# Kernel tuning notes

Measured on AMD Instinct MI355X. Metric: run time of the kernel, lower is better.

Reference implementation:

```python
import jax, jax.numpy as jnp
import numpy as np

B, T, H, K = 16, 8192, 256, 128
HQ = H // 4
NEG_INF = -jnp.inf


def setup_inputs() -> dict:
    key = jax.random.key(0)
    k1, k2, k3, k4, k5, k6, k7 = jax.random.split(key, 7)
    projected = jax.random.normal(k1, (B, T, H), dtype=jnp.float32)
    boundaries = jnp.sort(jax.random.randint(k2, (B, K, 2), 0, T), axis=-1)
    slot_mask = jax.random.randint(k3, (B, K), 0, 2, dtype=jnp.int32)
    # score_fn params: Linear(H, H//4) -> Tanh -> Linear(H//4, 1)
    s1 = 1.0 / np.sqrt(H)
    s2 = 1.0 / np.sqrt(HQ)
    W1 = jax.random.uniform(k4, (H, HQ), jnp.float32, -s1, s1)
    b1 = jax.random.uniform(k5, (HQ,), jnp.float32, -s1, s1)
    W2 = jax.random.uniform(k6, (HQ, 1), jnp.float32, -s2, s2)
    b2 = jax.random.uniform(k7, (1,), jnp.float32, -s2, s2)
    return {"projected": projected, "boundaries": boundaries, "slot_mask": slot_mask,
            "W1": W1, "b1": b1, "W2": W2, "b2": b2}


def reference(projected, boundaries, slot_mask, W1, b1, W2, b2):
    # scores: [B, T]
    h = jnp.tanh(projected @ W1 + b1)          # [B,T,HQ]
    scores = (h @ W2 + b2)[..., 0]             # [B,T]

    tidx = jnp.arange(T)[None, :, None]         # [1,T,1]
    starts = boundaries[:, None, :, 0]          # [B,1,K]
    ends = boundaries[:, None, :, 1]            # [B,1,K]
    in_slot = (tidx >= starts) & (tidx < ends) & (slot_mask[:, None, :] > 0)  # [B,T,K]

    # masked softmax over T, safe for fully-masked slots (torch yields 0 via masked_fill)
    s = scores[:, :, None]                      # [B,T,1] broadcast over K
    m = jnp.max(jnp.where(in_slot, s, NEG_INF), axis=1, keepdims=True)  # [B,1,K]
    m_safe = jnp.where(jnp.isfinite(m), m, 0.0)
    num = jnp.where(in_slot, jnp.exp(s - m_safe), 0.0)                  # [B,T,K]
    den = jnp.sum(num, axis=1, keepdims=True)                           # [B,1,K]
    w = num / jnp.where(den > 0, den, 1.0)                              # [B,T,K]

    return jnp.einsum('btk,bth->bkh', w, projected)                     # [B,K,H]
```

## Files before the change

kernel.cpp:

```cpp
#include <hip/hip_runtime.h>
#include <hip/hip_bf16.h>

#define BB 16
#define TT 8192
#define HH 256
#define KK 128
#define HQ 64

#define PT 64

typedef __attribute__((ext_vector_type(8))) short short8;
typedef __attribute__((ext_vector_type(4))) float f32x4;

__device__ inline unsigned short bf16_rne(float f) {
  unsigned u = __float_as_uint(f);
  unsigned r = u + 0x7FFF + ((u >> 16) & 1);
  return (unsigned short)(r >> 16);
}
__device__ inline float bf16_to_f(unsigned short h) {
  return __uint_as_float(((unsigned)h) << 16);
}

__global__ void prep_kernel(const float* __restrict__ W1,
                            unsigned short* __restrict__ Wp)
{
  int f = blockIdx.x * 256 + threadIdx.x;
  int e = f & 7;
  int l = (f >> 3) & 63;
  int n = (f >> 9) & 3;
  int s = f >> 11;
  int k = s * 32 + ((l >> 4) * 8) + e;
  int j = n * 16 + (l & 15);
  float w = W1[k * HQ + j];
  unsigned short hi = bf16_rne(w);
  Wp[f] = hi;
  Wp[16384 + f] = bf16_rne(w - bf16_to_f(hi));
}

__global__ __launch_bounds__(256, 2) void scores_mfma_kernel(
    const float* __restrict__ proj, const unsigned short* __restrict__ Wp,
    const float* __restrict__ b1, const float* __restrict__ W2,
    const float* __restrict__ b2, float* __restrict__ scores)
{
  __shared__ unsigned short Ahi[64][264];
  __shared__ unsigned short Alo[64][264];
  __shared__ float part[4][64];

  const int tid = threadIdx.x;
  const long long tile = blockIdx.x;
  const float4* src4 = (const float4*)(proj + tile * (64LL * HH));

  #pragma unroll
  for (int r = 0; r < 16; ++r) {
    int f = r * 256 + tid;
    int t = f >> 6;
    int c = f & 63;
    float4 v = src4[f];
    unsigned short h0 = bf16_rne(v.x), h1 = bf16_rne(v.y);
    unsigned short h2 = bf16_rne(v.z), h3 = bf16_rne(v.w);
    *(ushort4*)&Ahi[t][4 * c] = make_ushort4(h0, h1, h2, h3);
    *(ushort4*)&Alo[t][4 * c] = make_ushort4(bf16_rne(v.x - bf16_to_f(h0)),
                                             bf16_rne(v.y - bf16_to_f(h1)),
                                             bf16_rne(v.z - bf16_to_f(h2)),
                                             bf16_rne(v.w - bf16_to_f(h3)));
  }
  __syncthreads();

  const int w = tid >> 6;
  const int l = tid & 63;
  const int g = l >> 4;
  const int c = l & 15;

  f32x4 acc[4];
  #pragma unroll
  for (int m = 0; m < 4; ++m) acc[m] = (f32x4){0.f, 0.f, 0.f, 0.f};

  const short8* wp_hi = (const short8*)Wp;
  const short8* wp_lo = (const short8*)(Wp + 16384);

  #pragma unroll
  for (int s = 0; s < 8; ++s) {
    short8 bhi = wp_hi[(s * 4 + w) * 64 + l];
    short8 blo = wp_lo[(s * 4 + w) * 64 + l];
    #pragma unroll
    for (int m = 0; m < 4; ++m) {
      short8 ahi = *(const short8*)&Ahi[m * 16 + c][s * 32 + g * 8];
      short8 alo = *(const short8*)&Alo[m * 16 + c][s * 32 + g * 8];
      acc[m] = __builtin_amdgcn_mfma_f32_16x16x32_bf16(ahi, bhi, acc[m], 0, 0, 0);
      acc[m] = __builtin_amdgcn_mfma_f32_16x16x32_bf16(ahi, blo, acc[m], 0, 0, 0);
      acc[m] = __builtin_amdgcn_mfma_f32_16x16x32_bf16(alo, bhi, acc[m], 0, 0, 0);
    }
  }

  const int j = w * 16 + c;
  const float b1j = b1[j];
  const float w2j = W2[j];

  #pragma unroll
  for (int m = 0; m < 4; ++m) {
    #pragma unroll
    for (int r = 0; r < 4; ++r) {
      float x = tanhf(acc[m][r] + b1j) * w2j;
      x += __shfl_xor(x, 1);
      x += __shfl_xor(x, 2);
      x += __shfl_xor(x, 4);
      x += __shfl_xor(x, 8);
      if (c == r) part[w][m * 16 + g * 4 + r] = x;
    }
  }
  __syncthreads();

  if (tid < 64) {
    float s = part[0][tid] + part[1][tid] + part[2][tid] + part[3][tid] + b2[0];
    scores[tile * 64 + tid] = s;
  }
}

__global__ __launch_bounds__(256) void slotstats_kernel(
    const float* __restrict__ scores, const int* __restrict__ boundaries,
    const int* __restrict__ slot_mask, float* __restrict__ m_arr,
    float* __restrict__ invden)
{
  const int slot = blockIdx.x;
  const int b = slot >> 7;
  const int tid = threadIdx.x;
  const int st = boundaries[slot * 2 + 0];
  const int en = boundaries[slot * 2 + 1];
  const int mk = slot_mask[slot];
  __shared__ float red[4];

  if (mk <= 0 || en <= st) {
    if (tid == 0) { m_arr[slot] = 0.f; invden[slot] = 0.f; }
    return;
  }
  const float* sc = scores + (long long)b * TT;

  float mx = -3.4e38f;
  for (int t = st + tid; t < en; t += 256) mx = fmaxf(mx, sc[t]);
  #pragma unroll
  for (int o = 32; o > 0; o >>= 1) mx = fmaxf(mx, __shfl_xor(mx, o));
  if ((tid & 63) == 0) red[tid >> 6] = mx;
  __syncthreads();
  mx = fmaxf(fmaxf(red[0], red[1]), fmaxf(red[2], red[3]));
  __syncthreads();

  float se = 0.f;
  for (int t = st + tid; t < en; t += 256) se += expf(sc[t] - mx);
  #pragma unroll
  for (int o = 32; o > 0; o >>= 1) se += __shfl_xor(se, o);
  if ((tid & 63) == 0) red[tid >> 6] = se;
  __syncthreads();
  if (tid == 0) {
    m_arr[slot] = mx;
    invden[slot] = 1.f / (red[0] + red[1] + red[2] + red[3]);
  }
}

__global__ __launch_bounds__(512, 4) void pool_mfma_kernel(
    const float* __restrict__ proj, const float* __restrict__ scores,
    const int* __restrict__ boundaries, const float* __restrict__ m_arr,
    const float* __restrict__ invden, float* __restrict__ out)
{
  __shared__ unsigned short Bhi[256 * 64];
  __shared__ unsigned short Blo[256 * 64];
  __shared__ float s_lds[PT];
  __shared__ int   act_k[KK];
  __shared__ float act_m[KK], act_i[KK];
  __shared__ int   act_s[KK], act_e[KK];
  __shared__ int   nact;

  const int tid = threadIdx.x;
  const int b = blockIdx.y;
  const int t0 = blockIdx.x * PT;

  if (tid == 0) nact = 0;
  __syncthreads();

  if (tid < PT) s_lds[tid] = scores[(long long)b * TT + t0 + tid];
  if (tid < KK) {
    const int k = tid;
    const int st = boundaries[(b * KK + k) * 2 + 0];
    const int en = boundaries[(b * KK + k) * 2 + 1];
    const float inv = invden[b * KK + k];
    if (inv > 0.f && st < t0 + PT && en > t0) {
      int pos = atomicAdd(&nact, 1);
      act_k[pos] = k;
      act_m[pos] = m_arr[b * KK + k];
      act_i[pos] = inv;
      act_s[pos] = st;
      act_e[pos] = en;
    }
  }
  __syncthreads();
  const int na = nact;
  if (na == 0) return;

  {
    const int h = tid & 255;
    const int half = tid >> 8;
    const float* __restrict__ pcol =
        proj + ((long long)b * TT + t0 + half * 32) * HH + h;
    unsigned short* bh = &Bhi[h * 64];
    unsigned short* bl = &Blo[h * 64];
    const int hs = h & 7;
    #pragma unroll
    for (int o = 0; o < 4; ++o) {
      float v[8];
      #pragma unroll
      for (int i = 0; i < 8; ++i) v[i] = pcol[(o * 8 + i) * HH];
      short8 hv, lv;
      #pragma unroll
      for (int i = 0; i < 8; ++i) {
        unsigned short hi = bf16_rne(v[i]);
        hv[i] = (short)hi;
        lv[i] = (short)bf16_rne(v[i] - bf16_to_f(hi));
      }
      int cch = half * 4 + o;
      *(short8*)&bh[(cch ^ hs) << 3] = hv;
      *(short8*)&bl[(cch ^ hs) << 3] = lv;
    }
  }
  __syncthreads();

  const int l = tid & 63;
  const int w = tid >> 6;
  const int g = l >> 4;
  const int cl = l & 15;
  const int hbase = w * 32;

  for (int c0 = 0; c0 < na; c0 += 32) {
    f32x4 acc[2][2];
    #pragma unroll
    for (int m = 0; m < 2; ++m)
      #pragma unroll
      for (int nt = 0; nt < 2; ++nt) acc[m][nt] = (f32x4){0.f, 0.f, 0.f, 0.f};

    #pragma unroll
    for (int ksub = 0; ksub < 2; ++ksub) {
      float4 sv0 = *(const float4*)&s_lds[ksub * 32 + g * 8];
      float4 sv1 = *(const float4*)&s_lds[ksub * 32 + g * 8 + 4];
      float sv[8] = {sv0.x, sv0.y, sv0.z, sv0.w, sv1.x, sv1.y, sv1.z, sv1.w};

      short8 ahi[2], alo[2];
      #pragma unroll
      for (int m = 0; m < 2; ++m) {
        if (c0 + m * 16 < na) {
          int sidx = c0 + m * 16 + cl;
          bool act = sidx < na;
          int ix = act ? sidx : 0;
          float am = act_m[ix], ai = act_i[ix];
          int as = act_s[ix], ae = act_e[ix];
          #pragma unroll
          for (int e = 0; e < 8; ++e) {
            int t = t0 + ksub * 32 + g * 8 + e;
            float wgt = 0.f;
            if (act && t >= as && t < ae) wgt = expf(sv[e] - am) * ai;
            unsigned short hi = bf16_rne(wgt);
            ahi[m][e] = (short)hi;
            alo[m][e] = (short)bf16_rne(wgt - bf16_to_f(hi));
          }
        }
      }

      #pragma unroll
      for (int nt = 0; nt < 2; ++nt) {
        int hr = hbase + nt * 16 + cl;
        int cch = ksub * 4 + g;
        int off = hr * 64 + ((cch ^ (hr & 7)) << 3);
        short8 bhv = *(const short8*)&Bhi[off];
        short8 blv = *(const short8*)&Blo[off];
        #pragma unroll
        for (int m = 0; m < 2; ++m) {
          if (c0 + m * 16 < na) {
            acc[m][nt] = __builtin_amdgcn_mfma_f32_16x16x32_bf16(ahi[m], bhv, acc[m][nt], 0, 0, 0);
            acc[m][nt] = __builtin_amdgcn_mfma_f32_16x16x32_bf16(ahi[m], blv, acc[m][nt], 0, 0, 0);
            acc[m][nt] = __builtin_amdgcn_mfma_f32_16x16x32_bf16(alo[m], bhv, acc[m][nt], 0, 0, 0);
          }
        }
      }
    }

    #pragma unroll
    for (int m = 0; m < 2; ++m) {
      #pragma unroll
      for (int r = 0; r < 4; ++r) {
        int sc_i = c0 + m * 16 + g * 4 + r;
        if (sc_i < na) {
          long long obase = ((long long)(b * KK + act_k[sc_i])) * HH;
          #pragma unroll
          for (int nt = 0; nt < 2; ++nt)
            atomicAdd(out + obase + hbase + nt * 16 + cl, acc[m][nt][r]);
        }
      }
    }
  }
}

extern "C" void kernel_launch(void* const* d_in, const int* in_sizes, int n_in,
                              void* d_out, int out_size, void* d_ws, size_t ws_size,
                              hipStream_t stream)
{
  const float* proj       = (const float*)d_in[0];
  const int*   boundaries = (const int*)d_in[1];
  const int*   slot_mask  = (const int*)d_in[2];
  const float* W1         = (const float*)d_in[3];
  const float* b1         = (const float*)d_in[4];
  const float* W2         = (const float*)d_in[5];
  const float* b2         = (const float*)d_in[6];
  float* out = (float*)d_out;

  unsigned short* Wp = (unsigned short*)d_ws;
  float* scores = (float*)(Wp + 32768);
  float* m_arr  = scores + (size_t)BB * TT;
  float* invden = m_arr + BB * KK;

  hipMemsetAsync(d_out, 0, (size_t)out_size * sizeof(float), stream);

  prep_kernel<<<dim3(64), dim3(256), 0, stream>>>(W1, Wp);
  scores_mfma_kernel<<<dim3(BB * TT / 64), dim3(256), 0, stream>>>(
      proj, Wp, b1, W2, b2, scores);
  slotstats_kernel<<<dim3(BB * KK), dim3(256), 0, stream>>>(
      scores, boundaries, slot_mask, m_arr, invden);
  pool_mfma_kernel<<<dim3(TT / PT, BB), dim3(512), 0, stream>>>(
      proj, scores, boundaries, m_arr, invden, out);
}
```

Measured before the change: 312.4 us.

## Enlarge pool tile, stage softmax weights in LDS, use truncation splits and fast math

The pooling kernel now covers 128 timesteps per block with 1024 threads. Softmax weights are computed once per slot chunk into shared memory instead of being recomputed inside every wave, and each wave handles one 16-column slice of H. The high half of each bf16 split now uses bit truncation and the low half uses the packed convert intrinsic. tanh and exp switch to fast approximations. The larger tile halves the number of atomic outputs per slot, at the cost of heavier LDS use, extra barriers and lower occupancy.

```diff
diff --git a/kernel.cpp b/kernel.cpp
--- a/kernel.cpp
+++ b/kernel.cpp
@@ -7,7 +7,7 @@
 #define KK 128
 #define HQ 64
 
-#define PT 64
+#define PT 128
 
 typedef __attribute__((ext_vector_type(8))) short short8;
 typedef __attribute__((ext_vector_type(4))) float f32x4;
@@ -19,6 +19,16 @@
 }
 __device__ inline float bf16_to_f(unsigned short h) {
   return __uint_as_float(((unsigned)h) << 16);
+}
+__device__ inline unsigned cvtpk_bf16(float a, float b) {
+  union { __hip_bfloat162 h2; unsigned u; } cv;
+  cv.h2 = __float22bfloat162_rn(make_float2(a, b));
+  return cv.u;
+}
+__device__ inline float fast_tanh(float x) {
+  float t = __expf(-2.f * fabsf(x));
+  float r = (1.f - t) / (1.f + t);
+  return copysignf(r, x);
 }
 
 __global__ void prep_kernel(const float* __restrict__ W1,
@@ -56,13 +66,17 @@
     int t = f >> 6;
     int c = f & 63;
     float4 v = src4[f];
-    unsigned short h0 = bf16_rne(v.x), h1 = bf16_rne(v.y);
-    unsigned short h2 = bf16_rne(v.z), h3 = bf16_rne(v.w);
-    *(ushort4*)&Ahi[t][4 * c] = make_ushort4(h0, h1, h2, h3);
-    *(ushort4*)&Alo[t][4 * c] = make_ushort4(bf16_rne(v.x - bf16_to_f(h0)),
-                                             bf16_rne(v.y - bf16_to_f(h1)),
-                                             bf16_rne(v.z - bf16_to_f(h2)),
-                                             bf16_rne(v.w - bf16_to_f(h3)));
+    unsigned ux = __float_as_uint(v.x), uy = __float_as_uint(v.y);
+    unsigned uz = __float_as_uint(v.z), uw = __float_as_uint(v.w);
+    uint2 hi2 = make_uint2((ux >> 16) | (uy & 0xFFFF0000u),
+                           (uz >> 16) | (uw & 0xFFFF0000u));
+    float lx = v.x - __uint_as_float(ux & 0xFFFF0000u);
+    float ly = v.y - __uint_as_float(uy & 0xFFFF0000u);
+    float lz = v.z - __uint_as_float(uz & 0xFFFF0000u);
+    float lw = v.w - __uint_as_float(uw & 0xFFFF0000u);
+    uint2 lo2 = make_uint2(cvtpk_bf16(lx, ly), cvtpk_bf16(lz, lw));
+    *(uint2*)&Ahi[t][4 * c] = hi2;
+    *(uint2*)&Alo[t][4 * c] = lo2;
   }
   __syncthreads();
 
@@ -100,7 +114,7 @@
   for (int m = 0; m < 4; ++m) {
     #pragma unroll
     for (int r = 0; r < 4; ++r) {
-      float x = tanhf(acc[m][r] + b1j) * w2j;
+      float x = fast_tanh(acc[m][r] + b1j) * w2j;
       x += __shfl_xor(x, 1);
       x += __shfl_xor(x, 2);
       x += __shfl_xor(x, 4);
@@ -145,7 +159,7 @@
   __syncthreads();
 
   float se = 0.f;
-  for (int t = st + tid; t < en; t += 256) se += expf(sc[t] - mx);
+  for (int t = st + tid; t < en; t += 256) se += __expf(sc[t] - mx);
   #pragma unroll
   for (int o = 32; o > 0; o >>= 1) se += __shfl_xor(se, o);
   if ((tid & 63) == 0) red[tid >> 6] = se;
@@ -156,13 +170,14 @@
   }
 }
 
-__global__ __launch_bounds__(512, 4) void pool_mfma_kernel(
+__global__ __launch_bounds__(1024, 1) void pool_mfma_kernel(
     const float* __restrict__ proj, const float* __restrict__ scores,
     const int* __restrict__ boundaries, const float* __restrict__ m_arr,
     const float* __restrict__ invden, float* __restrict__ out)
 {
-  __shared__ unsigned short Bhi[256 * 64];
-  __shared__ unsigned short Blo[256 * 64];
+  __shared__ unsigned short Bhi[256 * PT];
+  __shared__ unsigned short Blo[256 * PT];
+  __shared__ unsigned short w_lds[2][32][PT];
   __shared__ float s_lds[PT];
   __shared__ int   act_k[KK];
   __shared__ float act_m[KK], act_i[KK];
@@ -191,91 +206,102 @@
       act_e[pos] = en;
     }
   }
-  __syncthreads();
-  const int na = nact;
-  if (na == 0) return;
 
   {
     const int h = tid & 255;
-    const int half = tid >> 8;
+    const int q = tid >> 8;
     const float* __restrict__ pcol =
-        proj + ((long long)b * TT + t0 + half * 32) * HH + h;
-    unsigned short* bh = &Bhi[h * 64];
-    unsigned short* bl = &Blo[h * 64];
+        proj + ((long long)b * TT + t0 + q * 32) * HH + h;
+    unsigned short* bh = &Bhi[h * PT];
+    unsigned short* bl = &Blo[h * PT];
     const int hs = h & 7;
     #pragma unroll
     for (int o = 0; o < 4; ++o) {
       float v[8];
       #pragma unroll
       for (int i = 0; i < 8; ++i) v[i] = pcol[(o * 8 + i) * HH];
-      short8 hv, lv;
+      unsigned hiw[4], low[4];
       #pragma unroll
-      for (int i = 0; i < 8; ++i) {
-        unsigned short hi = bf16_rne(v[i]);
-        hv[i] = (short)hi;
-        lv[i] = (short)bf16_rne(v[i] - bf16_to_f(hi));
-      }
-      int cch = half * 4 + o;
-      *(short8*)&bh[(cch ^ hs) << 3] = hv;
-      *(short8*)&bl[(cch ^ hs) << 3] = lv;
-    }
-  }
-  __syncthreads();
+      for (int i = 0; i < 4; ++i) {
+        unsigned u0 = __float_as_uint(v[2 * i]);
+        unsigned u1 = __float_as_uint(v[2 * i + 1]);
+        hiw[i] = (u0 >> 16) | (u1 & 0xFFFF0000u);
+        float l0 = v[2 * i] - __uint_as_float(u0 & 0xFFFF0000u);
+        float l1 = v[2 * i + 1] - __uint_as_float(u1 & 0xFFFF0000u);
+        low[i] = cvtpk_bf16(l0, l1);
+      }
+      int cch = (q * 4 + o) ^ hs;
+      *(uint4*)&bh[cch << 3] = make_uint4(hiw[0], hiw[1], hiw[2], hiw[3]);
+      *(uint4*)&bl[cch << 3] = make_uint4(low[0], low[1], low[2], low[3]);
+    }
+  }
+  __syncthreads();
+  const int na = nact;
+  if (na == 0) return;
 
   const int l = tid & 63;
   const int w = tid >> 6;
   const int g = l >> 4;
   const int cl = l & 15;
-  const int hbase = w * 32;
 
   for (int c0 = 0; c0 < na; c0 += 32) {
-    f32x4 acc[2][2];
-    #pragma unroll
-    for (int m = 0; m < 2; ++m)
-      #pragma unroll
-      for (int nt = 0; nt < 2; ++nt) acc[m][nt] = (f32x4){0.f, 0.f, 0.f, 0.f};
-
-    #pragma unroll
-    for (int ksub = 0; ksub < 2; ++ksub) {
-      float4 sv0 = *(const float4*)&s_lds[ksub * 32 + g * 8];
-      float4 sv1 = *(const float4*)&s_lds[ksub * 32 + g * 8 + 4];
-      float sv[8] = {sv0.x, sv0.y, sv0.z, sv0.w, sv1.x, sv1.y, sv1.z, sv1.w};
-
-      short8 ahi[2], alo[2];
+    {
+      const int which = tid >> 9;
+      const int s5 = (tid >> 4) & 31;
+      const int ch = tid & 15;
+      const int sg = c0 + s5;
+      float wv[8];
+      if (sg < na) {
+        const float am = act_m[sg], ai = act_i[sg];
+        const int as = act_s[sg], ae = act_e[sg];
+        #pragma unroll
+        for (int e = 0; e < 8; ++e) {
+          int t = t0 + ch * 8 + e;
+          wv[e] = (t >= as && t < ae) ? __expf(s_lds[ch * 8 + e] - am) * ai : 0.f;
+        }
+      } else {
+        #pragma unroll
+        for (int e = 0; e < 8; ++e) wv[e] = 0.f;
+      }
+      unsigned pk[4];
+      if (which == 0) {
+        #pragma unroll
+        for (int i = 0; i < 4; ++i)
+          pk[i] = (__float_as_uint(wv[2 * i]) >> 16) |
+                  (__float_as_uint(wv[2 * i + 1]) & 0xFFFF0000u);
+      } else {
+        #pragma unroll
+        for (int i = 0; i < 4; ++i) {
+          float l0 = wv[2 * i]     - __uint_as_float(__float_as_uint(wv[2 * i])     & 0xFFFF0000u);
+          float l1 = wv[2 * i + 1] - __uint_as_float(__float_as_uint(wv[2 * i + 1]) & 0xFFFF0000u);
+          pk[i] = cvtpk_bf16(l0, l1);
+        }
+      }
+      int swc = ch ^ (s5 & 7);
+      *(uint4*)&w_lds[which][s5][swc << 3] = make_uint4(pk[0], pk[1], pk[2], pk[3]);
+    }
+    __syncthreads();
+
+    f32x4 acc[2];
+    acc[0] = (f32x4){0.f, 0.f, 0.f, 0.f};
+    acc[1] = (f32x4){0.f, 0.f, 0.f, 0.f};
+
+    #pragma unroll
+    for (int ksub = 0; ksub < 4; ++ksub) {
+      const int hr = w * 16 + cl;
+      const int cch = (ksub * 4 + g) ^ (hr & 7);
+      short8 bhv = *(const short8*)&Bhi[hr * PT + (cch << 3)];
+      short8 blv = *(const short8*)&Blo[hr * PT + (cch << 3)];
       #pragma unroll
       for (int m = 0; m < 2; ++m) {
         if (c0 + m * 16 < na) {
-          int sidx = c0 + m * 16 + cl;
-          bool act = sidx < na;
-          int ix = act ? sidx : 0;
-          float am = act_m[ix], ai = act_i[ix];
-          int as = act_s[ix], ae = act_e[ix];
-          #pragma unroll
-          for (int e = 0; e < 8; ++e) {
-            int t = t0 + ksub * 32 + g * 8 + e;
-            float wgt = 0.f;
-            if (act && t >= as && t < ae) wgt = expf(sv[e] - am) * ai;
-            unsigned short hi = bf16_rne(wgt);
-            ahi[m][e] = (short)hi;
-            alo[m][e] = (short)bf16_rne(wgt - bf16_to_f(hi));
-          }
-        }
-      }
-
-      #pragma unroll
-      for (int nt = 0; nt < 2; ++nt) {
-        int hr = hbase + nt * 16 + cl;
-        int cch = ksub * 4 + g;
-        int off = hr * 64 + ((cch ^ (hr & 7)) << 3);
-        short8 bhv = *(const short8*)&Bhi[off];
-        short8 blv = *(const short8*)&Blo[off];
-        #pragma unroll
-        for (int m = 0; m < 2; ++m) {
-          if (c0 + m * 16 < na) {
-            acc[m][nt] = __builtin_amdgcn_mfma_f32_16x16x32_bf16(ahi[m], bhv, acc[m][nt], 0, 0, 0);
-            acc[m][nt] = __builtin_amdgcn_mfma_f32_16x16x32_bf16(ahi[m], blv, acc[m][nt], 0, 0, 0);
-            acc[m][nt] = __builtin_amdgcn_mfma_f32_16x16x32_bf16(alo[m], bhv, acc[m][nt], 0, 0, 0);
-          }
+          const int sl = m * 16 + cl;
+          const int swc = (ksub * 4 + g) ^ (sl & 7);
+          short8 ahi = *(const short8*)&w_lds[0][sl][swc << 3];
+          short8 alo = *(const short8*)&w_lds[1][sl][swc << 3];
+          acc[m] = __builtin_amdgcn_mfma_f32_16x16x32_bf16(ahi, bhv, acc[m], 0, 0, 0);
+          acc[m] = __builtin_amdgcn_mfma_f32_16x16x32_bf16(ahi, blv, acc[m], 0, 0, 0);
+          acc[m] = __builtin_amdgcn_mfma_f32_16x16x32_bf16(alo, bhv, acc[m], 0, 0, 0);
         }
       }
     }
@@ -287,12 +313,11 @@
         int sc_i = c0 + m * 16 + g * 4 + r;
         if (sc_i < na) {
           long long obase = ((long long)(b * KK + act_k[sc_i])) * HH;
-          #pragma unroll
-          for (int nt = 0; nt < 2; ++nt)
-            atomicAdd(out + obase + hbase + nt * 16 + cl, acc[m][nt][r]);
+          atomicAdd(out + obase + w * 16 + cl, acc[m][r]);
         }
       }
     }
+    __syncthreads();
   }
 }
 
@@ -321,6 +346,6 @@
       proj, Wp, b1, W2, b2, scores);
   slotstats_kernel<<<dim3(BB * KK), dim3(256), 0, stream>>>(
       scores, boundaries, slot_mask, m_arr, invden);
-  pool_mfma_kernel<<<dim3(TT / PT, BB), dim3(512), 0, stream>>>(
+  pool_mfma_kernel<<<dim3(TT / PT, BB), dim3(1024), 0, stream>>>(
       proj, scores, boundaries, m_arr, invden, out);
 }
```

Measured after the change: 278.9 us. -10.7%, faster.
